# Kernel tuning notes

Measured on AMD Instinct MI355X. Metric: run time of the kernel, lower is better.

## Reference

```python
import jax, jax.numpy as jnp
import numpy as np

TOP_K = 2  # num_experts_per_tok


def setup_inputs() -> dict:
    key = jax.random.key(0)
    ks = jax.random.split(key, 4)
    B, S, H, I, E = 4, 2048, 2048, 4096, 8
    std = 0.02
    hidden_states = jax.random.normal(ks[0], (B, S, H), dtype=jnp.float32)
    gate_w = jax.random.normal(ks[1], (E, H), dtype=jnp.float32) * std   # nn.Linear weight [E,H]
    wfc = jax.random.normal(ks[2], (E, I, H), dtype=jnp.float32) * std   # c_fc weight [E,out,in]
    bfc = jnp.zeros((E, I), dtype=jnp.float32)                           # bias zero-init
    wproj = jax.random.normal(ks[3], (E, H, I), dtype=jnp.float32) * std # c_proj weight
    bproj = jnp.zeros((E, H), dtype=jnp.float32)
    return {"hidden_states": hidden_states, "gate_w": gate_w, "wfc": wfc,
            "bfc": bfc, "wproj": wproj, "bproj": bproj}


def reference(hidden_states, gate_w, wfc, bfc, wproj, bproj):
    B, S, H = hidden_states.shape
    E = wfc.shape[0]
    x = hidden_states.reshape(-1, H)                      # [T, H]
    router_logits = x @ gate_w.T                          # [T, E]
    top_vals, top_idx = jax.lax.top_k(router_logits, TOP_K)
    router_weights = jax.nn.softmax(top_vals.astype(jnp.float32), axis=-1).astype(x.dtype)  # [T, k]
    out = jnp.zeros_like(x)
    # Loop over the small fixed set of experts; each token contributes with its
    # combined gate weight for that expert (0 if not routed there). Same math as
    # the torch gather/grouped-GEMM/scatter-add path.
    for e in range(E):
        gate_e = jnp.sum(jnp.where(top_idx == e, router_weights, 0.0), axis=-1)  # [T]
        h = jax.nn.gelu(x @ wfc[e].T + bfc[e], approximate=False)                # [T, I]
        y = h @ wproj[e].T + bproj[e]                                            # [T, H]
        out = out + gate_e[:, None] * y
    return out.reshape(B, S, H), router_logits
```

## Files before the change

kernel.cpp:

```cpp
#include <hip/hip_runtime.h>
#include <hip/hip_bf16.h>
#include <math.h>

#define NT 8192
#define HD 2048
#define ID 4096
#define NE 8
#define MAXSLOT 17408
#define MAXRB 136

typedef __bf16 bf16x8 __attribute__((ext_vector_type(8)));
typedef float f32x4 __attribute__((ext_vector_type(4)));

__device__ __forceinline__ float bf2f(unsigned short u){
  union{unsigned u; float f;} v; v.u = ((unsigned)u) << 16; return v.f;
}

__device__ __forceinline__ void gload_lds16(const void* g, void* l){
  __builtin_amdgcn_global_load_lds((const __attribute__((address_space(1))) void*)g,
                                   (__attribute__((address_space(3))) void*)l, 16, 0, 0);
}

__global__ __launch_bounds__(256) void cvt_kernel(const float* __restrict__ in,
                                                  __hip_bfloat16* __restrict__ outp, int n4){
  int i = blockIdx.x * blockDim.x + threadIdx.x;
  int stride = gridDim.x * blockDim.x;
  for (; i < n4; i += stride){
    float4 v = reinterpret_cast<const float4*>(in)[i];
    union{ushort4 u; __hip_bfloat16 h[4];} o;
    o.h[0] = __float2bfloat16(v.x); o.h[1] = __float2bfloat16(v.y);
    o.h[2] = __float2bfloat16(v.z); o.h[3] = __float2bfloat16(v.w);
    reinterpret_cast<ushort4*>(outp)[i] = o.u;
  }
}

__global__ __launch_bounds__(256) void router_kernel(
    const float* __restrict__ x, const float* __restrict__ gw,
    float* __restrict__ logits_out, int* __restrict__ tokExp,
    float* __restrict__ tokW, int* __restrict__ cnt)
{
  int wave = (blockIdx.x * blockDim.x + threadIdx.x) >> 6;
  int lane = threadIdx.x & 63;
  if (wave >= NT) return;
  const float* xr = x + (long)wave * HD;
  double acc[NE];
  #pragma unroll
  for (int e = 0; e < NE; e++) acc[e] = 0.0;
  for (int k = lane; k < HD; k += 64){
    double xv = (double)xr[k];
    #pragma unroll
    for (int e = 0; e < NE; e++) acc[e] += xv * (double)gw[e * HD + k];
  }
  #pragma unroll
  for (int e = 0; e < NE; e++){
    #pragma unroll
    for (int off = 32; off; off >>= 1) acc[e] += __shfl_down(acc[e], off, 64);
  }
  if (lane == 0){
    int e0 = 0; double v0 = acc[0];
    for (int e = 1; e < NE; e++) if (acc[e] > v0){ v0 = acc[e]; e0 = e; }
    int e1 = -1; double v1 = -1e300;
    for (int e = 0; e < NE; e++) if (e != e0 && acc[e] > v1){ v1 = acc[e]; e1 = e; }
    double ex = exp(v1 - v0);
    double s = 1.0 + ex;
    for (int e = 0; e < NE; e++) logits_out[wave * NE + e] = (float)acc[e];
    tokExp[wave * 2]     = e0; tokExp[wave * 2 + 1] = e1;
    tokW[wave * 2]       = (float)(1.0 / s);
    tokW[wave * 2 + 1]   = (float)(ex / s);
    atomicAdd(&cnt[e0], 1); atomicAdd(&cnt[e1], 1);
  }
}

__global__ void offsets_kernel(const int* __restrict__ cnt, int* __restrict__ padOff){
  if (threadIdx.x == 0 && blockIdx.x == 0){
    int o = 0;
    for (int e = 0; e < NE; e++){ padOff[e] = o; o += ((cnt[e] + 127) >> 7) << 7; }
    padOff[NE] = o;
  }
}

__global__ __launch_bounds__(256) void scatter_kernel(
    const int* __restrict__ tokExp, const float* __restrict__ tokW,
    const int* __restrict__ padOff, int* cursor,
    int* __restrict__ slotTok, int* __restrict__ tokSlot)
{
  int t = blockIdx.x * blockDim.x + threadIdx.x;
  if (t >= NT) return;
  #pragma unroll
  for (int s = 0; s < 2; s++){
    int e = tokExp[t * 2 + s];
    int pos = atomicAdd(&cursor[e], 1);
    int slot = padOff[e] + pos;
    slotTok[slot] = t;
    tokSlot[t * 2 + s] = slot;
  }
}

template<int GATHER_A, int EPI, int ND, int KD>
__global__ __launch_bounds__(256, 2) void moe_gemm(
    const __hip_bfloat16* __restrict__ A,
    const float* __restrict__ W,
    const float* __restrict__ bias,
    const int* __restrict__ slotTok,
    const int* __restrict__ padOff,
    __hip_bfloat16* __restrict__ Yout)
{
  __shared__ __hip_bfloat16 As[128 * 32];
  __shared__ __hip_bfloat16 Bs[128 * 32];
  const int rb = blockIdx.y;
  const int total = padOff[NE];
  if (rb * 128 >= total) return;
  const int cb = blockIdx.x;
  int e = 0;
  #pragma unroll
  for (int i = 1; i < NE; i++) if (rb * 128 >= padOff[i]) e = i;

  const int tid  = threadIdx.x;
  const int lane = tid & 63;
  const int w    = tid >> 6;
  const int wr   = w >> 1, wc = w & 1;

  const int j0  = 2 * w;
  const int ar0 = j0 * 16 + (lane >> 2);
  const int kch = lane & 3;
  long aRow0, aRow1;
  {
    int g0 = rb * 128 + ar0, g1 = g0 + 16;
    if (GATHER_A){
      int t0 = slotTok[g0]; if (t0 < 0) t0 = 0;
      int t1 = slotTok[g1]; if (t1 < 0) t1 = 0;
      aRow0 = t0; aRow1 = t1;
    } else { aRow0 = g0; aRow1 = g1; }
  }
  const __hip_bfloat16* gA0 = A + aRow0 * (long)KD + kch * 8;
  const __hip_bfloat16* gA1 = A + aRow1 * (long)KD + kch * 8;
  __hip_bfloat16* lA0 = &As[j0 * 512];
  __hip_bfloat16* lA1 = &As[j0 * 512 + 512];

  const float* gB = W + (long)e * ND * KD + ((long)cb * 128 + (tid >> 3)) * KD + (tid & 7) * 4;
  __hip_bfloat16* lB = &Bs[(tid >> 3) * 32 + (tid & 7) * 4];

  const int frow = lane & 15;
  const int fkb  = (lane >> 4) * 8;
  const bf16x8* aP[4]; const bf16x8* bP[4];
  #pragma unroll
  for (int m = 0; m < 4; m++) aP[m] = reinterpret_cast<const bf16x8*>(&As[(wr * 64 + m * 16 + frow) * 32 + fkb]);
  #pragma unroll
  for (int n = 0; n < 4; n++) bP[n] = reinterpret_cast<const bf16x8*>(&Bs[(wc * 64 + n * 16 + frow) * 32 + fkb]);

  f32x4 acc[4][4] = {};

  const int NKS = KD / 32;
  for (int kt = 0; kt < NKS; kt++){
    __syncthreads();
    gload_lds16(gA0 + kt * 32, lA0);
    gload_lds16(gA1 + kt * 32, lA1);
    #pragma unroll
    for (int q = 0; q < 4; q++){
      float4 v = *reinterpret_cast<const float4*>(gB + (long)q * 32 * KD + kt * 32);
      union{ushort4 u; __hip_bfloat16 h[4];} pk;
      pk.h[0] = __float2bfloat16(v.x); pk.h[1] = __float2bfloat16(v.y);
      pk.h[2] = __float2bfloat16(v.z); pk.h[3] = __float2bfloat16(v.w);
      *reinterpret_cast<ushort4*>(lB + q * 32 * 32) = pk.u;
    }
    __syncthreads();
    bf16x8 av[4], bv[4];
    #pragma unroll
    for (int m = 0; m < 4; m++) av[m] = aP[m][0];
    #pragma unroll
    for (int n = 0; n < 4; n++) bv[n] = bP[n][0];
    #pragma unroll
    for (int m = 0; m < 4; m++){
      #pragma unroll
      for (int n = 0; n < 4; n++){
        acc[m][n] = __builtin_amdgcn_mfma_f32_16x16x32_bf16(av[m], bv[n], acc[m][n], 0, 0, 0);
      }
    }
  }

  const int col0 = cb * 128 + wc * 64 + frow;
  const int row0 = rb * 128 + wr * 64 + (lane >> 4) * 4;
  #pragma unroll
  for (int n = 0; n < 4; n++){
    const int col = col0 + n * 16;
    const float bb = bias[(long)e * ND + col];
    #pragma unroll
    for (int m = 0; m < 4; m++){
      const long rbase = (long)(row0 + m * 16);
      #pragma unroll
      for (int r = 0; r < 4; r++){
        float v = acc[m][n][r] + bb;
        if (EPI == 0){
          v = 0.5f * v * (1.0f + erff(v * 0.70710678118654752f));
        }
        Yout[(rbase + r) * ND + col] = __float2bfloat16(v);
      }
    }
  }
}

__global__ __launch_bounds__(256) void combine_kernel(
    const __hip_bfloat16* __restrict__ yb,
    const int* __restrict__ tokSlot, const float* __restrict__ tokW,
    float* __restrict__ outp)
{
  const int t  = blockIdx.x;
  const int c0 = threadIdx.x * 8;
  const int s0 = tokSlot[t * 2], s1 = tokSlot[t * 2 + 1];
  const float w0 = tokW[t * 2], w1 = tokW[t * 2 + 1];
  const ushort4* p0 = reinterpret_cast<const ushort4*>(yb + (long)s0 * HD + c0);
  const ushort4* p1 = reinterpret_cast<const ushort4*>(yb + (long)s1 * HD + c0);
  float4 o[2];
  #pragma unroll
  for (int h = 0; h < 2; h++){
    ushort4 a = p0[h], b = p1[h];
    o[h].x = w0 * bf2f(a.x) + w1 * bf2f(b.x);
    o[h].y = w0 * bf2f(a.y) + w1 * bf2f(b.y);
    o[h].z = w0 * bf2f(a.z) + w1 * bf2f(b.z);
    o[h].w = w0 * bf2f(a.w) + w1 * bf2f(b.w);
  }
  float4* po = reinterpret_cast<float4*>(outp + (long)t * HD + c0);
  po[0] = o[0]; po[1] = o[1];
}

extern "C" void kernel_launch(void* const* d_in, const int* in_sizes, int n_in,
                              void* d_out, int out_size, void* d_ws, size_t ws_size,
                              hipStream_t stream)
{
  (void)in_sizes; (void)n_in; (void)out_size; (void)ws_size;
  const float* x     = (const float*)d_in[0];
  const float* gw    = (const float*)d_in[1];
  const float* wfc   = (const float*)d_in[2];
  const float* bfc   = (const float*)d_in[3];
  const float* wproj = (const float*)d_in[4];
  const float* bproj = (const float*)d_in[5];
  float* outp   = (float*)d_out;
  float* logits = outp + (size_t)NT * HD;

  char* ws = (char*)d_ws;
  size_t off = 0;
  auto alloc = [&](size_t b){ void* p = ws + off; off += (b + 255) & ~(size_t)255; return p; };

  char* shared0 = (char*)alloc((size_t)MAXSLOT * HD * 2);
  __hip_bfloat16* xb = (__hip_bfloat16*)shared0;
  __hip_bfloat16* yb = (__hip_bfloat16*)shared0;
  __hip_bfloat16* hb = (__hip_bfloat16*)alloc((size_t)MAXSLOT * ID * 2);
  int*   slotTok = (int*)alloc(MAXSLOT * 4);
  int*   tokExp  = (int*)alloc(NT * 2 * 4);
  float* tokW    = (float*)alloc(NT * 2 * 4);
  int*   tokSlot = (int*)alloc(NT * 2 * 4);
  int*   meta    = (int*)alloc(256);
  int* cnt = meta; int* cursor = meta + 8; int* padOff = meta + 16;

  hipMemsetAsync(meta, 0, 256, stream);
  hipMemsetAsync(slotTok, 0xFF, MAXSLOT * 4, stream);

  cvt_kernel<<<2048, 256, 0, stream>>>(x, xb, NT * HD / 4);
  router_kernel<<<NT / 4, 256, 0, stream>>>(x, gw, logits, tokExp, tokW, cnt);
  offsets_kernel<<<1, 64, 0, stream>>>(cnt, padOff);
  scatter_kernel<<<NT / 256, 256, 0, stream>>>(tokExp, tokW, padOff, cursor, slotTok, tokSlot);
  moe_gemm<1, 0, ID, HD><<<dim3(ID / 128, MAXRB), 256, 0, stream>>>(xb, wfc, bfc, slotTok, padOff, hb);
  moe_gemm<0, 1, HD, ID><<<dim3(HD / 128, MAXRB), 256, 0, stream>>>(hb, wproj, bproj, slotTok, padOff, yb);
  combine_kernel<<<NT, 256, 0, stream>>>(yb, tokSlot, tokW, outp);
}
```

Measured before the change: 1.266 ms.

## Pre-convert expert weights to bf16 and stream them via direct LDS loads

Adds a pass that converts each expert weight tensor to bf16 in workspace before its GEMM. The GEMM then loads weights with global_load_lds, as it already does for activations, instead of loading fp32 and converting per tile in registers. This removes redundant per-block conversion and halves the weight bytes each tile reads. The cost is an extra full read and write of 256MB of fp32 weights per GEMM, plus a 128MB workspace requirement. When the workspace is too small it falls back to the old fp32-weight kernel. The occupancy hint is also raised to 4 blocks per CU.

```diff
diff --git a/kernel.cpp b/kernel.cpp
--- a/kernel.cpp
+++ b/kernel.cpp
@@ -97,9 +97,9 @@
 }
 
 template<int GATHER_A, int EPI, int ND, int KD>
-__global__ __launch_bounds__(256, 2) void moe_gemm(
+__global__ __launch_bounds__(256, 4) void moe_gemm_bf(
     const __hip_bfloat16* __restrict__ A,
-    const float* __restrict__ W,
+    const __hip_bfloat16* __restrict__ W,
     const float* __restrict__ bias,
     const int* __restrict__ slotTok,
     const int* __restrict__ padOff,
@@ -137,8 +137,11 @@
   __hip_bfloat16* lA0 = &As[j0 * 512];
   __hip_bfloat16* lA1 = &As[j0 * 512 + 512];
 
-  const float* gB = W + (long)e * ND * KD + ((long)cb * 128 + (tid >> 3)) * KD + (tid & 7) * 4;
-  __hip_bfloat16* lB = &Bs[(tid >> 3) * 32 + (tid & 7) * 4];
+  const long bRow0 = (long)cb * 128 + ar0;
+  const __hip_bfloat16* gB0 = W + (long)e * ND * KD + bRow0 * KD + kch * 8;
+  const __hip_bfloat16* gB1 = gB0 + 16 * (long)KD;
+  __hip_bfloat16* lB0 = &Bs[j0 * 512];
+  __hip_bfloat16* lB1 = &Bs[j0 * 512 + 512];
 
   const int frow = lane & 15;
   const int fkb  = (lane >> 4) * 8;
@@ -155,14 +158,8 @@
     __syncthreads();
     gload_lds16(gA0 + kt * 32, lA0);
     gload_lds16(gA1 + kt * 32, lA1);
-    #pragma unroll
-    for (int q = 0; q < 4; q++){
-      float4 v = *reinterpret_cast<const float4*>(gB + (long)q * 32 * KD + kt * 32);
-      union{ushort4 u; __hip_bfloat16 h[4];} pk;
-      pk.h[0] = __float2bfloat16(v.x); pk.h[1] = __float2bfloat16(v.y);
-      pk.h[2] = __float2bfloat16(v.z); pk.h[3] = __float2bfloat16(v.w);
-      *reinterpret_cast<ushort4*>(lB + q * 32 * 32) = pk.u;
-    }
+    gload_lds16(gB0 + kt * 32, lB0);
+    gload_lds16(gB1 + kt * 32, lB1);
     __syncthreads();
     bf16x8 av[4], bv[4];
     #pragma unroll
@@ -199,6 +196,109 @@
   }
 }
 
+template<int GATHER_A, int EPI, int ND, int KD>
+__global__ __launch_bounds__(256, 2) void moe_gemm_f32(
+    const __hip_bfloat16* __restrict__ A,
+    const float* __restrict__ W,
+    const float* __restrict__ bias,
+    const int* __restrict__ slotTok,
+    const int* __restrict__ padOff,
+    __hip_bfloat16* __restrict__ Yout)
+{
+  __shared__ __hip_bfloat16 As[128 * 32];
+  __shared__ __hip_bfloat16 Bs[128 * 32];
+  const int rb = blockIdx.y;
+  const int total = padOff[NE];
+  if (rb * 128 >= total) return;
+  const int cb = blockIdx.x;
+  int e = 0;
+  #pragma unroll
+  for (int i = 1; i < NE; i++) if (rb * 128 >= padOff[i]) e = i;
+
+  const int tid  = threadIdx.x;
+  const int lane = tid & 63;
+  const int w    = tid >> 6;
+  const int wr   = w >> 1, wc = w & 1;
+
+  const int j0  = 2 * w;
+  const int ar0 = j0 * 16 + (lane >> 2);
+  const int kch = lane & 3;
+  long aRow0, aRow1;
+  {
+    int g0 = rb * 128 + ar0, g1 = g0 + 16;
+    if (GATHER_A){
+      int t0 = slotTok[g0]; if (t0 < 0) t0 = 0;
+      int t1 = slotTok[g1]; if (t1 < 0) t1 = 0;
+      aRow0 = t0; aRow1 = t1;
+    } else { aRow0 = g0; aRow1 = g1; }
+  }
+  const __hip_bfloat16* gA0 = A + aRow0 * (long)KD + kch * 8;
+  const __hip_bfloat16* gA1 = A + aRow1 * (long)KD + kch * 8;
+  __hip_bfloat16* lA0 = &As[j0 * 512];
+  __hip_bfloat16* lA1 = &As[j0 * 512 + 512];
+
+  const float* gB = W + (long)e * ND * KD + ((long)cb * 128 + (tid >> 3)) * KD + (tid & 7) * 4;
+  __hip_bfloat16* lB = &Bs[(tid >> 3) * 32 + (tid & 7) * 4];
+
+  const int frow = lane & 15;
+  const int fkb  = (lane >> 4) * 8;
+  const bf16x8* aP[4]; const bf16x8* bP[4];
+  #pragma unroll
+  for (int m = 0; m < 4; m++) aP[m] = reinterpret_cast<const bf16x8*>(&As[(wr * 64 + m * 16 + frow) * 32 + fkb]);
+  #pragma unroll
+  for (int n = 0; n < 4; n++) bP[n] = reinterpret_cast<const bf16x8*>(&Bs[(wc * 64 + n * 16 + frow) * 32 + fkb]);
+
+  f32x4 acc[4][4] = {};
+
+  const int NKS = KD / 32;
+  for (int kt = 0; kt < NKS; kt++){
+    __syncthreads();
+    gload_lds16(gA0 + kt * 32, lA0);
+    gload_lds16(gA1 + kt * 32, lA1);
+    #pragma unroll
+    for (int q = 0; q < 4; q++){
+      float4 v = *reinterpret_cast<const float4*>(gB + (long)q * 32 * KD + kt * 32);
+      union{ushort4 u; __hip_bfloat16 h[4];} pk;
+      pk.h[0] = __float2bfloat16(v.x); pk.h[1] = __float2bfloat16(v.y);
+      pk.h[2] = __float2bfloat16(v.z); pk.h[3] = __float2bfloat16(v.w);
+      *reinterpret_cast<ushort4*>(lB + q * 32 * 32) = pk.u;
+    }
+    __syncthreads();
+    bf16x8 av[4], bv[4];
+    #pragma unroll
+    for (int m = 0; m < 4; m++) av[m] = aP[m][0];
+    #pragma unroll
+    for (int n = 0; n < 4; n++) bv[n] = bP[n][0];
+    #pragma unroll
+    for (int m = 0; m < 4; m++){
+      #pragma unroll
+      for (int n = 0; n < 4; n++){
+        acc[m][n] = __builtin_amdgcn_mfma_f32_16x16x32_bf16(av[m], bv[n], acc[m][n], 0, 0, 0);
+      }
+    }
+  }
+
+  const int col0 = cb * 128 + wc * 64 + frow;
+  const int row0 = rb * 128 + wr * 64 + (lane >> 4) * 4;
+  #pragma unroll
+  for (int n = 0; n < 4; n++){
+    const int col = col0 + n * 16;
+    const float bb = bias[(long)e * ND + col];
+    #pragma unroll
+    for (int m = 0; m < 4; m++){
+      const long rbase = (long)(row0 + m * 16);
+      #pragma unroll
+      for (int r = 0; r < 4; r++){
+        float v = acc[m][n][r] + bb;
+        if (EPI == 0){
+          v = 0.5f * v * (1.0f + erff(v * 0.70710678118654752f));
+        }
+        Yout[(rbase + r) * ND + col] = __float2bfloat16(v);
+      }
+    }
+  }
+}
+
 __global__ __launch_bounds__(256) void combine_kernel(
     const __hip_bfloat16* __restrict__ yb,
     const int* __restrict__ tokSlot, const float* __restrict__ tokW,
@@ -227,7 +327,7 @@
                               void* d_out, int out_size, void* d_ws, size_t ws_size,
                               hipStream_t stream)
 {
-  (void)in_sizes; (void)n_in; (void)out_size; (void)ws_size;
+  (void)in_sizes; (void)n_in; (void)out_size;
   const float* x     = (const float*)d_in[0];
   const float* gw    = (const float*)d_in[1];
   const float* wfc   = (const float*)d_in[2];
@@ -252,6 +352,10 @@
   int*   meta    = (int*)alloc(256);
   int* cnt = meta; int* cursor = meta + 8; int* padOff = meta + 16;
 
+  const size_t WB_BYTES = (size_t)NE * ID * HD * 2;
+  __hip_bfloat16* wB = (__hip_bfloat16*)(ws + off);
+  const bool pre = (off + WB_BYTES) <= ws_size;
+
   hipMemsetAsync(meta, 0, 256, stream);
   hipMemsetAsync(slotTok, 0xFF, MAXSLOT * 4, stream);
 
@@ -259,7 +363,16 @@
   router_kernel<<<NT / 4, 256, 0, stream>>>(x, gw, logits, tokExp, tokW, cnt);
   offsets_kernel<<<1, 64, 0, stream>>>(cnt, padOff);
   scatter_kernel<<<NT / 256, 256, 0, stream>>>(tokExp, tokW, padOff, cursor, slotTok, tokSlot);
-  moe_gemm<1, 0, ID, HD><<<dim3(ID / 128, MAXRB), 256, 0, stream>>>(xb, wfc, bfc, slotTok, padOff, hb);
-  moe_gemm<0, 1, HD, ID><<<dim3(HD / 128, MAXRB), 256, 0, stream>>>(hb, wproj, bproj, slotTok, padOff, yb);
+
+  if (pre){
+    cvt_kernel<<<2048, 256, 0, stream>>>(wfc, wB, NE * ID * HD / 4);
+    moe_gemm_bf<1, 0, ID, HD><<<dim3(ID / 128, MAXRB), 256, 0, stream>>>(xb, wB, bfc, slotTok, padOff, hb);
+    cvt_kernel<<<2048, 256, 0, stream>>>(wproj, wB, NE * HD * ID / 4);
+    moe_gemm_bf<0, 1, HD, ID><<<dim3(HD / 128, MAXRB), 256, 0, stream>>>(hb, wB, bproj, slotTok, padOff, yb);
+  } else {
+    moe_gemm_f32<1, 0, ID, HD><<<dim3(ID / 128, MAXRB), 256, 0, stream>>>(xb, wfc, bfc, slotTok, padOff, hb);
+    moe_gemm_f32<0, 1, HD, ID><<<dim3(HD / 128, MAXRB), 256, 0, stream>>>(hb, wproj, bproj, slotTok, padOff, yb);
+  }
+
   combine_kernel<<<NT, 256, 0, stream>>>(yb, tokSlot, tokW, outp);
 }
```

Measured after the change: 1.253 ms. No clear change (-1.0%).

## Rewrite MoE GEMM as 256x256 double-buffered bf16 tiles with pre-converted weights

Applied to the files above, without the earlier changes.

Each expert's fp32 weights are now converted to bf16 into a workspace buffer before its GEMM, so both operands stream into LDS through direct global-to-LDS loads. The GEMM uses a 256x256 tile with 512 threads, a double-buffered and XOR-swizzled LDS pipeline, and split-phase barriers with raised MFMA priority, to overlap loads with matrix math. The down-projection epilogue writes rows directly at token*2+slot positions, so combine reads them contiguously and the tokSlot indirection goes away. In exchange, each call adds two full weight-conversion passes over memory, uses 128KB of LDS per block, and pads expert groups to 256 rows, which wastes more compute.

```diff
diff --git a/kernel.cpp b/kernel.cpp
--- a/kernel.cpp
+++ b/kernel.cpp
@@ -6,8 +6,8 @@
 #define HD 2048
 #define ID 4096
 #define NE 8
-#define MAXSLOT 17408
-#define MAXRB 136
+#define MAXSLOT 18432
+#define MAXRB 72
 
 typedef __bf16 bf16x8 __attribute__((ext_vector_type(8)));
 typedef float f32x4 __attribute__((ext_vector_type(4)));
@@ -74,15 +74,14 @@
 __global__ void offsets_kernel(const int* __restrict__ cnt, int* __restrict__ padOff){
   if (threadIdx.x == 0 && blockIdx.x == 0){
     int o = 0;
-    for (int e = 0; e < NE; e++){ padOff[e] = o; o += ((cnt[e] + 127) >> 7) << 7; }
+    for (int e = 0; e < NE; e++){ padOff[e] = o; o += ((cnt[e] + 255) >> 8) << 8; }
     padOff[NE] = o;
   }
 }
 
 __global__ __launch_bounds__(256) void scatter_kernel(
-    const int* __restrict__ tokExp, const float* __restrict__ tokW,
-    const int* __restrict__ padOff, int* cursor,
-    int* __restrict__ slotTok, int* __restrict__ tokSlot)
+    const int* __restrict__ tokExp, const int* __restrict__ padOff, int* cursor,
+    int* __restrict__ slotTok)
 {
   int t = blockIdx.x * blockDim.x + threadIdx.x;
   if (t >= NT) return;
@@ -90,126 +89,198 @@
   for (int s = 0; s < 2; s++){
     int e = tokExp[t * 2 + s];
     int pos = atomicAdd(&cursor[e], 1);
-    int slot = padOff[e] + pos;
-    slotTok[slot] = t;
-    tokSlot[t * 2 + s] = slot;
-  }
-}
-
-template<int GATHER_A, int EPI, int ND, int KD>
-__global__ __launch_bounds__(256, 2) void moe_gemm(
+    slotTok[padOff[e] + pos] = t * 2 + s;
+  }
+}
+
+
+#define LDA(buf,kk,m) (*reinterpret_cast<const bf16x8*>(&lds[((buf)*2+(kk))*8192 + (wr*8+(m))*512 + laneF]))
+#define LDB(buf,kk,n) (*reinterpret_cast<const bf16x8*>(&lds[32768 + ((buf)*2+(kk))*8192 + (wc*4+(n))*512 + laneF]))
+#define STAGE_A(buf,kk,koff) do{ \
+    __hip_bfloat16* d_ = &lds[((buf)*2+(kk))*8192 + w*1024]; \
+    gload_lds16(aS0 + (koff), d_); \
+    gload_lds16(aS1 + (koff), d_ + 512); \
+  }while(0)
+#define STAGE_B(buf,kk,koff) do{ \
+    __hip_bfloat16* d_ = &lds[32768 + ((buf)*2+(kk))*8192 + w*1024]; \
+    gload_lds16(bS0 + (koff), d_); \
+    gload_lds16(bS1 + (koff), d_ + 512); \
+  }while(0)
+#define MFMA16(M0,A0_,A1_,A2_,A3_) do{ \
+    acc[(M0)+0][0] = __builtin_amdgcn_mfma_f32_16x16x32_bf16(A0_, bv0, acc[(M0)+0][0],0,0,0); \
+    acc[(M0)+1][0] = __builtin_amdgcn_mfma_f32_16x16x32_bf16(A1_, bv0, acc[(M0)+1][0],0,0,0); \
+    acc[(M0)+2][0] = __builtin_amdgcn_mfma_f32_16x16x32_bf16(A2_, bv0, acc[(M0)+2][0],0,0,0); \
+    acc[(M0)+3][0] = __builtin_amdgcn_mfma_f32_16x16x32_bf16(A3_, bv0, acc[(M0)+3][0],0,0,0); \
+    acc[(M0)+0][1] = __builtin_amdgcn_mfma_f32_16x16x32_bf16(A0_, bv1, acc[(M0)+0][1],0,0,0); \
+    acc[(M0)+1][1] = __builtin_amdgcn_mfma_f32_16x16x32_bf16(A1_, bv1, acc[(M0)+1][1],0,0,0); \
+    acc[(M0)+2][1] = __builtin_amdgcn_mfma_f32_16x16x32_bf16(A2_, bv1, acc[(M0)+2][1],0,0,0); \
+    acc[(M0)+3][1] = __builtin_amdgcn_mfma_f32_16x16x32_bf16(A3_, bv1, acc[(M0)+3][1],0,0,0); \
+    acc[(M0)+0][2] = __builtin_amdgcn_mfma_f32_16x16x32_bf16(A0_, bv2, acc[(M0)+0][2],0,0,0); \
+    acc[(M0)+1][2] = __builtin_amdgcn_mfma_f32_16x16x32_bf16(A1_, bv2, acc[(M0)+1][2],0,0,0); \
+    acc[(M0)+2][2] = __builtin_amdgcn_mfma_f32_16x16x32_bf16(A2_, bv2, acc[(M0)+2][2],0,0,0); \
+    acc[(M0)+3][2] = __builtin_amdgcn_mfma_f32_16x16x32_bf16(A3_, bv2, acc[(M0)+3][2],0,0,0); \
+    acc[(M0)+0][3] = __builtin_amdgcn_mfma_f32_16x16x32_bf16(A0_, bv3, acc[(M0)+0][3],0,0,0); \
+    acc[(M0)+1][3] = __builtin_amdgcn_mfma_f32_16x16x32_bf16(A1_, bv3, acc[(M0)+1][3],0,0,0); \
+    acc[(M0)+2][3] = __builtin_amdgcn_mfma_f32_16x16x32_bf16(A2_, bv3, acc[(M0)+3][3],0,0,0); \
+    acc[(M0)+3][3] = __builtin_amdgcn_mfma_f32_16x16x32_bf16(A3_, bv3, acc[(M0)+3][3],0,0,0); \
+  }while(0)
+
+#undef MFMA16
+#define MFMA16(M0,A0_,A1_,A2_,A3_) do{ \
+    acc[(M0)+0][0] = __builtin_amdgcn_mfma_f32_16x16x32_bf16(A0_, bv0, acc[(M0)+0][0],0,0,0); \
+    acc[(M0)+1][0] = __builtin_amdgcn_mfma_f32_16x16x32_bf16(A1_, bv0, acc[(M0)+1][0],0,0,0); \
+    acc[(M0)+2][0] = __builtin_amdgcn_mfma_f32_16x16x32_bf16(A2_, bv0, acc[(M0)+2][0],0,0,0); \
+    acc[(M0)+3][0] = __builtin_amdgcn_mfma_f32_16x16x32_bf16(A3_, bv0, acc[(M0)+3][0],0,0,0); \
+    acc[(M0)+0][1] = __builtin_amdgcn_mfma_f32_16x16x32_bf16(A0_, bv1, acc[(M0)+0][1],0,0,0); \
+    acc[(M0)+1][1] = __builtin_amdgcn_mfma_f32_16x16x32_bf16(A1_, bv1, acc[(M0)+1][1],0,0,0); \
+    acc[(M0)+2][1] = __builtin_amdgcn_mfma_f32_16x16x32_bf16(A2_, bv1, acc[(M0)+2][1],0,0,0); \
+    acc[(M0)+3][1] = __builtin_amdgcn_mfma_f32_16x16x32_bf16(A3_, bv1, acc[(M0)+3][1],0,0,0); \
+    acc[(M0)+0][2] = __builtin_amdgcn_mfma_f32_16x16x32_bf16(A0_, bv2, acc[(M0)+0][2],0,0,0); \
+    acc[(M0)+1][2] = __builtin_amdgcn_mfma_f32_16x16x32_bf16(A1_, bv2, acc[(M0)+1][2],0,0,0); \
+    acc[(M0)+2][2] = __builtin_amdgcn_mfma_f32_16x16x32_bf16(A2_, bv2, acc[(M0)+2][2],0,0,0); \
+    acc[(M0)+3][2] = __builtin_amdgcn_mfma_f32_16x16x32_bf16(A3_, bv2, acc[(M0)+3][2],0,0,0); \
+    acc[(M0)+0][3] = __builtin_amdgcn_mfma_f32_16x16x32_bf16(A0_, bv3, acc[(M0)+0][3],0,0,0); \
+    acc[(M0)+1][3] = __builtin_amdgcn_mfma_f32_16x16x32_bf16(A1_, bv3, acc[(M0)+1][3],0,0,0); \
+    acc[(M0)+2][3] = __builtin_amdgcn_mfma_f32_16x16x32_bf16(A2_, bv3, acc[(M0)+2][3],0,0,0); \
+    acc[(M0)+3][3] = __builtin_amdgcn_mfma_f32_16x16x32_bf16(A3_, bv3, acc[(M0)+3][3],0,0,0); \
+  }while(0)
+
+template<int GDIV, int EPI, int ND, int KD>
+__global__ __launch_bounds__(512, 2) void moe_gemm8(
     const __hip_bfloat16* __restrict__ A,
-    const float* __restrict__ W,
+    const __hip_bfloat16* __restrict__ W,
     const float* __restrict__ bias,
     const int* __restrict__ slotTok,
     const int* __restrict__ padOff,
     __hip_bfloat16* __restrict__ Yout)
 {
-  __shared__ __hip_bfloat16 As[128 * 32];
-  __shared__ __hip_bfloat16 Bs[128 * 32];
+  __shared__ __align__(16) __hip_bfloat16 lds[65536];
   const int rb = blockIdx.y;
-  const int total = padOff[NE];
-  if (rb * 128 >= total) return;
+  if (rb * 256 >= padOff[NE]) return;
   const int cb = blockIdx.x;
   int e = 0;
   #pragma unroll
-  for (int i = 1; i < NE; i++) if (rb * 128 >= padOff[i]) e = i;
+  for (int i = 1; i < NE; i++) if (rb * 256 >= padOff[i]) e = i;
 
   const int tid  = threadIdx.x;
   const int lane = tid & 63;
   const int w    = tid >> 6;
-  const int wr   = w >> 1, wc = w & 1;
-
-  const int j0  = 2 * w;
-  const int ar0 = j0 * 16 + (lane >> 2);
-  const int kch = lane & 3;
-  long aRow0, aRow1;
-  {
-    int g0 = rb * 128 + ar0, g1 = g0 + 16;
-    if (GATHER_A){
-      int t0 = slotTok[g0]; if (t0 < 0) t0 = 0;
-      int t1 = slotTok[g1]; if (t1 < 0) t1 = 0;
-      aRow0 = t0; aRow1 = t1;
-    } else { aRow0 = g0; aRow1 = g1; }
-  }
-  const __hip_bfloat16* gA0 = A + aRow0 * (long)KD + kch * 8;
-  const __hip_bfloat16* gA1 = A + aRow1 * (long)KD + kch * 8;
-  __hip_bfloat16* lA0 = &As[j0 * 512];
-  __hip_bfloat16* lA1 = &As[j0 * 512 + 512];
-
-  const float* gB = W + (long)e * ND * KD + ((long)cb * 128 + (tid >> 3)) * KD + (tid & 7) * 4;
-  __hip_bfloat16* lB = &Bs[(tid >> 3) * 32 + (tid & 7) * 4];
-
-  const int frow = lane & 15;
-  const int fkb  = (lane >> 4) * 8;
-  const bf16x8* aP[4]; const bf16x8* bP[4];
-  #pragma unroll
-  for (int m = 0; m < 4; m++) aP[m] = reinterpret_cast<const bf16x8*>(&As[(wr * 64 + m * 16 + frow) * 32 + fkb]);
-  #pragma unroll
-  for (int n = 0; n < 4; n++) bP[n] = reinterpret_cast<const bf16x8*>(&Bs[(wc * 64 + n * 16 + frow) * 32 + fkb]);
-
-  f32x4 acc[4][4] = {};
-
-  const int NKS = KD / 32;
-  for (int kt = 0; kt < NKS; kt++){
-    __syncthreads();
-    gload_lds16(gA0 + kt * 32, lA0);
-    gload_lds16(gA1 + kt * 32, lA1);
+  const int wr   = w >> 2;
+  const int wc   = w & 3;
+
+  const int r16s = lane >> 2;
+  const int cgs  = (lane & 3) ^ ((r16s >> 1) & 3);
+  const int rowA = rb * 256 + 32 * w + r16s;
+  int pr0 = slotTok[rowA];      long ga0 = pr0 < 0 ? 0 : (pr0 >> GDIV);
+  int pr1 = slotTok[rowA + 16]; long ga1 = pr1 < 0 ? 0 : (pr1 >> GDIV);
+  const __hip_bfloat16* aS0 = A + ga0 * (long)KD + cgs * 8;
+  const __hip_bfloat16* aS1 = A + ga1 * (long)KD + cgs * 8;
+  const long rowB = (long)cb * 256 + 32 * w + r16s;
+  const __hip_bfloat16* bS0 = W + (long)e * ND * KD + rowB * KD + cgs * 8;
+  const __hip_bfloat16* bS1 = bS0 + 16 * (long)KD;
+
+  const int r16f = lane & 15;
+  const int chf  = lane >> 4;
+  const int laneF = r16f * 32 + (chf ^ ((r16f >> 1) & 3)) * 8;
+
+  f32x4 acc[8][4] = {};
+  bf16x8 bv0, bv1, bv2, bv3;
+
+  constexpr int NTILES = KD / 64;
+
+  STAGE_A(0,0,0);   STAGE_B(0,0,0);
+  STAGE_A(0,1,32);  STAGE_B(0,1,32);
+  STAGE_A(1,0,64);  STAGE_B(1,0,64);
+  STAGE_A(1,1,96);  STAGE_B(1,1,96);
+  asm volatile("s_waitcnt vmcnt(8)" ::: "memory");
+  __builtin_amdgcn_s_barrier();
+
+  for (int t = 0; t < NTILES; ++t){
+    const int b = t & 1;
+    const bool s01 = (t >= 1) && (t + 1 < NTILES);
+    const bool s23 = (t + 2 < NTILES);
+    const long ko01 = (long)(t + 1) * 64 + 32;
+    const long ko23 = (long)(t + 2) * 64;
+    {
+      bf16x8 a0 = LDA(b,0,0), a1 = LDA(b,0,1), a2 = LDA(b,0,2), a3 = LDA(b,0,3);
+      bv0 = LDB(b,0,0); bv1 = LDB(b,0,1); bv2 = LDB(b,0,2); bv3 = LDB(b,0,3);
+      if (s01){ STAGE_A(b^1,1,ko01); }
+      __builtin_amdgcn_s_barrier();
+      asm volatile("s_waitcnt lgkmcnt(0)" ::: "memory");
+      __builtin_amdgcn_s_setprio(1);
+      MFMA16(0, a0, a1, a2, a3);
+      __builtin_amdgcn_s_setprio(0);
+      __builtin_amdgcn_s_barrier();
+    }
+    {
+      bf16x8 a0 = LDA(b,0,4), a1 = LDA(b,0,5), a2 = LDA(b,0,6), a3 = LDA(b,0,7);
+      if (s01){ STAGE_B(b^1,1,ko01); }
+      __builtin_amdgcn_s_barrier();
+      asm volatile("s_waitcnt lgkmcnt(0)" ::: "memory");
+      __builtin_amdgcn_s_setprio(1);
+      MFMA16(4, a0, a1, a2, a3);
+      __builtin_amdgcn_s_setprio(0);
+      __builtin_amdgcn_s_barrier();
+    }
+    {
+      bf16x8 a0 = LDA(b,1,0), a1 = LDA(b,1,1), a2 = LDA(b,1,2), a3 = LDA(b,1,3);
+      bv0 = LDB(b,1,0); bv1 = LDB(b,1,1); bv2 = LDB(b,1,2); bv3 = LDB(b,1,3);
+      if (s23){ STAGE_A(b,0,ko23); }
+      __builtin_amdgcn_s_barrier();
+      asm volatile("s_waitcnt lgkmcnt(0)" ::: "memory");
+      __builtin_amdgcn_s_setprio(1);
+      MFMA16(0, a0, a1, a2, a3);
+      __builtin_amdgcn_s_setprio(0);
+      __builtin_amdgcn_s_barrier();
+    }
+    {
+      bf16x8 a0 = LDA(b,1,4), a1 = LDA(b,1,5), a2 = LDA(b,1,6), a3 = LDA(b,1,7);
+      if (s23){ STAGE_B(b,0,ko23); }
+      __builtin_amdgcn_s_barrier();
+      asm volatile("s_waitcnt lgkmcnt(0)" ::: "memory");
+      __builtin_amdgcn_s_setprio(1);
+      MFMA16(4, a0, a1, a2, a3);
+      __builtin_amdgcn_s_setprio(0);
+      if (s23) asm volatile("s_waitcnt vmcnt(4)" ::: "memory");
+      else     asm volatile("s_waitcnt vmcnt(0)" ::: "memory");
+      __builtin_amdgcn_s_barrier();
+    }
+  }
+
+  const int colBase = cb * 256 + wc * 64 + (lane & 15);
+  const int rowQ = (lane >> 4) * 4;
+  float bb[4];
+  #pragma unroll
+  for (int n = 0; n < 4; n++) bb[n] = bias[(long)e * ND + colBase + n * 16];
+  #pragma unroll
+  for (int m = 0; m < 8; m++){
+    const int grow = rb * 256 + wr * 128 + m * 16 + rowQ;
     #pragma unroll
-    for (int q = 0; q < 4; q++){
-      float4 v = *reinterpret_cast<const float4*>(gB + (long)q * 32 * KD + kt * 32);
-      union{ushort4 u; __hip_bfloat16 h[4];} pk;
-      pk.h[0] = __float2bfloat16(v.x); pk.h[1] = __float2bfloat16(v.y);
-      pk.h[2] = __float2bfloat16(v.z); pk.h[3] = __float2bfloat16(v.w);
-      *reinterpret_cast<ushort4*>(lB + q * 32 * 32) = pk.u;
-    }
-    __syncthreads();
-    bf16x8 av[4], bv[4];
-    #pragma unroll
-    for (int m = 0; m < 4; m++) av[m] = aP[m][0];
-    #pragma unroll
-    for (int n = 0; n < 4; n++) bv[n] = bP[n][0];
-    #pragma unroll
-    for (int m = 0; m < 4; m++){
-      #pragma unroll
-      for (int n = 0; n < 4; n++){
-        acc[m][n] = __builtin_amdgcn_mfma_f32_16x16x32_bf16(av[m], bv[n], acc[m][n], 0, 0, 0);
+    for (int r = 0; r < 4; r++){
+      const int pr = slotTok[grow + r];
+      if (pr >= 0){
+        #pragma unroll
+        for (int n = 0; n < 4; n++){
+          float v = acc[m][n][r] + bb[n];
+          if (EPI == 0){
+            v = 0.5f * v * (1.0f + erff(v * 0.70710678118654752f));
+          }
+          Yout[(long)pr * ND + colBase + n * 16] = __float2bfloat16(v);
+        }
       }
     }
   }
-
-  const int col0 = cb * 128 + wc * 64 + frow;
-  const int row0 = rb * 128 + wr * 64 + (lane >> 4) * 4;
-  #pragma unroll
-  for (int n = 0; n < 4; n++){
-    const int col = col0 + n * 16;
-    const float bb = bias[(long)e * ND + col];
-    #pragma unroll
-    for (int m = 0; m < 4; m++){
-      const long rbase = (long)(row0 + m * 16);
-      #pragma unroll
-      for (int r = 0; r < 4; r++){
-        float v = acc[m][n][r] + bb;
-        if (EPI == 0){
-          v = 0.5f * v * (1.0f + erff(v * 0.70710678118654752f));
-        }
-        Yout[(rbase + r) * ND + col] = __float2bfloat16(v);
-      }
-    }
-  }
 }
 
 __global__ __launch_bounds__(256) void combine_kernel(
-    const __hip_bfloat16* __restrict__ yb,
-    const int* __restrict__ tokSlot, const float* __restrict__ tokW,
+    const __hip_bfloat16* __restrict__ yb, const float* __restrict__ tokW,
     float* __restrict__ outp)
 {
   const int t  = blockIdx.x;
   const int c0 = threadIdx.x * 8;
-  const int s0 = tokSlot[t * 2], s1 = tokSlot[t * 2 + 1];
   const float w0 = tokW[t * 2], w1 = tokW[t * 2 + 1];
-  const ushort4* p0 = reinterpret_cast<const ushort4*>(yb + (long)s0 * HD + c0);
-  const ushort4* p1 = reinterpret_cast<const ushort4*>(yb + (long)s1 * HD + c0);
+  const ushort4* p0 = reinterpret_cast<const ushort4*>(yb + (long)(2 * t) * HD + c0);
+  const ushort4* p1 = reinterpret_cast<const ushort4*>(yb + (long)(2 * t + 1) * HD + c0);
   float4 o[2];
   #pragma unroll
   for (int h = 0; h < 2; h++){
@@ -241,14 +312,14 @@
   size_t off = 0;
   auto alloc = [&](size_t b){ void* p = ws + off; off += (b + 255) & ~(size_t)255; return p; };
 
-  char* shared0 = (char*)alloc((size_t)MAXSLOT * HD * 2);
-  __hip_bfloat16* xb = (__hip_bfloat16*)shared0;
-  __hip_bfloat16* yb = (__hip_bfloat16*)shared0;
-  __hip_bfloat16* hb = (__hip_bfloat16*)alloc((size_t)MAXSLOT * ID * 2);
+  char* region0 = (char*)alloc((size_t)NT * 2 * HD * 2);
+  __hip_bfloat16* xb = (__hip_bfloat16*)region0;
+  __hip_bfloat16* yb = (__hip_bfloat16*)region0;
+  __hip_bfloat16* hb = (__hip_bfloat16*)alloc((size_t)NT * 2 * ID * 2);
+  __hip_bfloat16* wB = (__hip_bfloat16*)alloc((size_t)NE * ID * HD * 2);
   int*   slotTok = (int*)alloc(MAXSLOT * 4);
   int*   tokExp  = (int*)alloc(NT * 2 * 4);
   float* tokW    = (float*)alloc(NT * 2 * 4);
-  int*   tokSlot = (int*)alloc(NT * 2 * 4);
   int*   meta    = (int*)alloc(256);
   int* cnt = meta; int* cursor = meta + 8; int* padOff = meta + 16;
 
@@ -258,8 +329,12 @@
   cvt_kernel<<<2048, 256, 0, stream>>>(x, xb, NT * HD / 4);
   router_kernel<<<NT / 4, 256, 0, stream>>>(x, gw, logits, tokExp, tokW, cnt);
   offsets_kernel<<<1, 64, 0, stream>>>(cnt, padOff);
-  scatter_kernel<<<NT / 256, 256, 0, stream>>>(tokExp, tokW, padOff, cursor, slotTok, tokSlot);
-  moe_gemm<1, 0, ID, HD><<<dim3(ID / 128, MAXRB), 256, 0, stream>>>(xb, wfc, bfc, slotTok, padOff, hb);
-  moe_gemm<0, 1, HD, ID><<<dim3(HD / 128, MAXRB), 256, 0, stream>>>(hb, wproj, bproj, slotTok, padOff, yb);
-  combine_kernel<<<NT, 256, 0, stream>>>(yb, tokSlot, tokW, outp);
-}
+  scatter_kernel<<<NT / 256, 256, 0, stream>>>(tokExp, padOff, cursor, slotTok);
+
+  cvt_kernel<<<2048, 256, 0, stream>>>(wfc, wB, NE * ID * HD / 4);
+  moe_gemm8<1, 0, ID, HD><<<dim3(ID / 256, MAXRB), 512, 0, stream>>>(xb, wB, bfc, slotTok, padOff, hb);
+  cvt_kernel<<<2048, 256, 0, stream>>>(wproj, wB, NE * HD * ID / 4);
+  moe_gemm8<0, 1, HD, ID><<<dim3(HD / 256, MAXRB), 512, 0, stream>>>(hb, wB, bproj, slotTok, padOff, yb);
+
+  combine_kernel<<<NT, 256, 0, stream>>>(yb, tokW, outp);
+}
```

New measurement: 1.230 ms. 2.8% less time.
